# Kernel tuning notes

Hardware: AMD Instinct MI355X
Metric: run time of the kernel (lower is better)

Reference implementation:

```python
import jax, jax.numpy as jnp
import numpy as np

B, T, N, H = 512, 128, 256, 256  # batch, time_step, input_size, hidden_size


def setup_inputs() -> dict:
    key = jax.random.key(0)
    ks = jax.random.split(key, 8)
    s_lin = 1.0 / np.sqrt(T)
    s_ih = 1.0 / np.sqrt(H)
    return {
        "X": jax.random.normal(ks[0], (B, T, N), dtype=jnp.float32),
        "Wq": jax.random.uniform(ks[1], (T, T), jnp.float32, -s_lin, s_lin),
        "Wk": jax.random.uniform(ks[2], (T, T), jnp.float32, -s_lin, s_lin),
        "Wv": jax.random.uniform(ks[3], (T, T), jnp.float32, -s_lin, s_lin),
        "W_ih": jax.random.uniform(ks[4], (4 * H, N), jnp.float32, -s_ih, s_ih),
        "W_hh": jax.random.uniform(ks[5], (4 * H, H), jnp.float32, -s_ih, s_ih),
        "b_ih": jax.random.uniform(ks[6], (4 * H,), jnp.float32, -s_ih, s_ih),
        "b_hh": jax.random.uniform(ks[7], (4 * H,), jnp.float32, -s_ih, s_ih),
    }


def _forward(X, Wq, Wk, Wv, W_ih, W_hh, b_ih, b_hh):
    b, t, n = X.shape
    Xp = jnp.swapaxes(X, 1, 2)  # (B, N, T)
    Q = Xp @ Wq.T               # (B, N, T)
    K = Xp @ Wk.T               # (B, N, T)
    V = Xp @ Wv.T               # (B, N, T)
    # QK[b,i,j] = sum_t Q[b,i,t] * K[b,j,t]; scale by sqrt(N)
    scores = jnp.einsum('bit,bjt->bij', Q, K) / jnp.sqrt(jnp.float32(n))
    A = jax.nn.softmax(scores, axis=-1)          # (B, N, N)
    Xa = jnp.einsum('bij,bjt->bit', A, V)        # (B, N, T)
    Xa = jnp.swapaxes(Xa, 1, 2)                  # (B, T, N)

    h0 = jnp.zeros((b, W_hh.shape[1]), X.dtype)
    c0 = h0

    def step(carry, x_t):
        h, c = carry
        gates = x_t @ W_ih.T + b_ih + h @ W_hh.T + b_hh  # (B, 4H)
        i, f, g, o = jnp.split(gates, 4, axis=-1)         # PyTorch gate order
        i = jax.nn.sigmoid(i)
        f = jax.nn.sigmoid(f)
        g = jnp.tanh(g)
        o = jax.nn.sigmoid(o)
        c = f * c + i * g
        h = o * jnp.tanh(c)
        return (h, c), h

    _, hs = jax.lax.scan(step, (h0, c0), jnp.swapaxes(Xa, 0, 1))  # (T, B, H)
    return jnp.swapaxes(hs, 0, 1)  # (B, T, H)


def reference(X, Wq, Wk, Wv, W_ih, W_hh, b_ih, b_hh):
    return _forward(X, Wq, Wk, Wv, W_ih, W_hh, b_ih, b_hh)
```

## Files before the change

kernel.cpp:

```cpp
#include <hip/hip_runtime.h>
#include <hip/hip_bf16.h>
#include <stdint.h>


#define DI __device__ __forceinline__

typedef __attribute__((ext_vector_type(8))) short bf16x8;
typedef __attribute__((ext_vector_type(4))) short short4v;
typedef __attribute__((ext_vector_type(4))) float f32x4;
typedef __attribute__((ext_vector_type(4))) int int4v;

union U8 { bf16x8 v; short4v h[2]; int4v i; };

DI unsigned short f2bf(float x){
  union { float f; unsigned u; } v; v.f = x;
  unsigned r = v.u + 0x7fffu + ((v.u >> 16) & 1u);
  return (unsigned short)(r >> 16);
}
DI float bf2f(unsigned short x){
  union { unsigned u; float f; } v; v.u = ((unsigned)x) << 16; return v.f;
}
DI float rcp_(float x){ return __builtin_amdgcn_rcpf(x); }
DI float sigm(float x){ return rcp_(1.0f + __expf(-x)); }
DI float tanhf_(float x){ return 1.0f - 2.0f * rcp_(1.0f + __expf(2.0f * x)); }

#define BB 512
#define TT 128
#define NN 256
#define HH 256

__global__ void k_prep3(const float* __restrict__ Wq, const float* __restrict__ Wk,
                        const float* __restrict__ Wv, const float* __restrict__ Wih,
                        const float* __restrict__ Whh,
                        const float* __restrict__ bih, const float* __restrict__ bhh,
                        unsigned short* __restrict__ wqb, unsigned short* __restrict__ wkb,
                        unsigned short* __restrict__ wvb,
                        unsigned short* __restrict__ wihf, unsigned short* __restrict__ whhf,
                        float* __restrict__ bias, int* __restrict__ flags){
  int bx = blockIdx.x;
  if (bx < 64){
    int i = bx * 256 + threadIdx.x;
    wqb[i] = f2bf(Wq[i]); wkb[i] = f2bf(Wk[i]); wvb[i] = f2bf(Wv[i]);
    if (i < 1024) bias[i] = bih[i] + bhh[i];
    if (i < 256) flags[i] = 0;
    return;
  }
  const float* W = (bx < 96) ? Whh : Wih;
  unsigned short* w_f = (bx < 96) ? whhf : wihf;
  int idx = ((bx < 96) ? (bx - 64) : (bx - 96)) * 256 + threadIdx.x;
  int j = idx >> 3, kk = idx & 7;
  const float* src = W + j * 256 + kk * 32;
  unsigned short o[32];
  #pragma unroll
  for (int g = 0; g < 4; ++g)
    #pragma unroll
    for (int e = 0; e < 4; ++e){
      o[g * 8 + e]     = f2bf(src[4 * g + e]);
      o[g * 8 + 4 + e] = f2bf(src[16 + 4 * g + e]);
    }
  int4v* dst = (int4v*)((char*)w_f + j * 512 + kk * 64);
  #pragma unroll
  for (int q = 0; q < 4; ++q) dst[q] = *(int4v*)(o + q * 8);
}

__global__ __launch_bounds__(256) void k_qkv2(const float* __restrict__ X,
      const unsigned short* __restrict__ Wqb, const unsigned short* __restrict__ Wkb,
      const unsigned short* __restrict__ Wvb,
      unsigned short* __restrict__ Qo, unsigned short* __restrict__ Ko,
      unsigned short* __restrict__ Vo){
  __shared__ __align__(16) char smem[98816];
  char* As2 = smem;
  float* tile = (float*)(smem + 32768);
  char* Bs = smem + 32768;
  char* Os = smem + 65536;
  int bid = blockIdx.x;
  int b = bid >> 1, nh = bid & 1;
  int n0 = nh * 128;
  int m0 = b * 256 + n0;
  int tid = threadIdx.x;

  {
    int nl = tid & 127, tg = tid >> 7;
    const float* src = X + (size_t)b * TT * NN + n0 + nl;
    #pragma unroll
    for (int r = 0; r < 64; ++r){
      int t = r * 2 + tg;
      tile[t * 129 + nl] = src[(size_t)t * NN];
    }
  }
  __syncthreads();
  {
    int tpos = tid & 31, nrow = tid >> 5;
    #pragma unroll
    for (int rr = 0; rr < 16; ++rr){
      int n = rr * 8 + nrow;
      int t0 = tpos * 4;
      short4v v = { (short)f2bf(tile[(t0    ) * 129 + n]),
                    (short)f2bf(tile[(t0 + 1) * 129 + n]),
                    (short)f2bf(tile[(t0 + 2) * 129 + n]),
                    (short)f2bf(tile[(t0 + 3) * 129 + n]) };
      *(short4v*)(As2 + n * 256 + ((t0 * 2) ^ ((n & 7) << 4))) = v;
    }
  }

  int lane = tid & 63, wv = tid >> 6;
  int wr = wv >> 1, wc = wv & 1;
  int l15 = lane & 15, g = lane >> 4;
  f32x4 zro = {0.f, 0.f, 0.f, 0.f};

  #pragma unroll 1
  for (int mode = 0; mode < 3; ++mode){
    const unsigned short* W = (mode == 0) ? Wqb : ((mode == 1) ? Wkb : Wvb);
    __syncthreads();
    #pragma unroll
    for (int it = 0; it < 16; ++it){
      int c = it * 256 + tid;
      int j = c >> 5;
      int kc = (c & 31) << 2;
      short4v v = *(const short4v*)(W + j * 128 + kc);
      *(short4v*)(Bs + j * 256 + ((kc * 2) ^ ((j & 7) << 4))) = v;
    }
    __syncthreads();
    f32x4 acc[4][4];
    #pragma unroll
    for (int a = 0; a < 4; ++a)
      #pragma unroll
      for (int bq = 0; bq < 4; ++bq) acc[a][bq] = zro;
    #pragma unroll
    for (int ks = 0; ks < 4; ++ks){
      U8 af[4];
      #pragma unroll
      for (int mt = 0; mt < 4; ++mt){
        int ar = wr * 64 + mt * 16 + l15;
        const char* ab = As2 + ar * 256;
        int sw = (ar & 7) << 4;
        af[mt].h[0] = *(const short4v*)(ab + ((ks * 64 + 8 * g) ^ sw));
        af[mt].h[1] = *(const short4v*)(ab + ((ks * 64 + 8 * g + 32) ^ sw));
      }
      #pragma unroll
      for (int nt = 0; nt < 4; ++nt){
        int jr = wc * 64 + nt * 16 + l15;
        const char* bb = Bs + jr * 256;
        int kb = ks * 64 + 8 * g, sw = (jr & 7) << 4;
        U8 bf;
        bf.h[0] = *(const short4v*)(bb + (kb ^ sw));
        bf.h[1] = *(const short4v*)(bb + ((kb + 32) ^ sw));
        #pragma unroll
        for (int mt = 0; mt < 4; ++mt)
          acc[mt][nt] = __builtin_amdgcn_mfma_f32_16x16x32_bf16(af[mt].v, bf.v, acc[mt][nt], 0, 0, 0);
      }
    }
    float scale = (mode == 0) ? 0.0625f : 1.0f;
    #pragma unroll
    for (int mt = 0; mt < 4; ++mt)
      #pragma unroll
      for (int nt = 0; nt < 4; ++nt)
        #pragma unroll
        for (int r = 0; r < 4; ++r){
          int row = wr * 64 + mt * 16 + g * 4 + r;
          int col = wc * 64 + nt * 16 + l15;
          unsigned short hv = f2bf(acc[mt][nt][r] * scale);
          int addr = (mode == 2) ? (col * 256 + ((row * 2) ^ ((col & 7) << 4)))
                                 : (row * 256 + ((col * 2) ^ ((row & 7) << 4)));
          *(unsigned short*)(Os + addr) = hv;
        }
    __syncthreads();
    int orow = tid >> 1, oseg = tid & 1;
    const char* srcrow = Os + orow * 256;
    unsigned short* dst;
    if (mode == 2){
      dst = Vo + ((size_t)b * 128 + orow) * 256 + n0 + oseg * 64;
    } else {
      dst = ((mode == 0) ? Qo : Ko) + (size_t)(m0 + orow) * 128 + oseg * 64;
    }
    #pragma unroll
    for (int c = 0; c < 8; ++c){
      int kb = oseg * 128 + c * 16;
      *(int4v*)((char*)dst + c * 16) = *(const int4v*)(srcrow + (kb ^ ((orow & 7) << 4)));
    }
  }
}

__global__ __launch_bounds__(512) void k_attn2(const unsigned short* __restrict__ Q,
        const unsigned short* __restrict__ K, const unsigned short* __restrict__ Vt,
        unsigned short* __restrict__ Xa){
  __shared__ __align__(16) char smem[131072 + 512];
  char* Qs = smem;
  char* Ks = smem + 32768;
  char* Ps = smem;
  char* Vs = smem + 65536;
  float* rden = (float*)(smem + 131072);
  int b = blockIdx.y, i0 = blockIdx.x * 128;
  int tid = threadIdx.x, lane = tid & 63, wv = tid >> 6;
  int l15 = lane & 15, g = lane >> 4;

  {
    int row = tid >> 2, q = tid & 3;
    const char* src = (const char*)(Q + ((size_t)b * 256 + i0 + row) * 128) + q * 64;
    char* dstr = Qs + row * 256;
    int sw = (row & 7) << 4;
    #pragma unroll
    for (int c = 0; c < 4; ++c){
      int kb = q * 64 + c * 16;
      *(int4v*)(dstr + (kb ^ sw)) = *(const int4v*)(src + c * 16);
    }
  }
  {
    int row = tid >> 1, half = tid & 1;
    const char* src = (const char*)(K + ((size_t)b * 256 + row) * 128) + half * 128;
    char* dstr = Ks + row * 256;
    int sw = (row & 7) << 4;
    #pragma unroll
    for (int c = 0; c < 8; ++c){
      int kb = half * 128 + c * 16;
      *(int4v*)(dstr + (kb ^ sw)) = *(const int4v*)(src + c * 16);
    }
  }
  __syncthreads();

  f32x4 zro = {0.f, 0.f, 0.f, 0.f};
  f32x4 acc[16];
  #pragma unroll
  for (int nt = 0; nt < 16; ++nt) acc[nt] = zro;
  #pragma unroll
  for (int kk = 0; kk < 4; ++kk){
    int ar = wv * 16 + l15;
    const char* ab = Qs + ar * 256;
    int kb = kk * 64 + 8 * g, swa = (ar & 7) << 4;
    U8 a;
    a.h[0] = *(const short4v*)(ab + (kb ^ swa));
    a.h[1] = *(const short4v*)(ab + ((kb + 32) ^ swa));
    #pragma unroll
    for (int nt = 0; nt < 16; ++nt){
      int jr = nt * 16 + l15;
      const char* bb = Ks + jr * 256;
      int swb = (jr & 7) << 4;
      U8 bf;
      bf.h[0] = *(const short4v*)(bb + (kb ^ swb));
      bf.h[1] = *(const short4v*)(bb + ((kb + 32) ^ swb));
      acc[nt] = __builtin_amdgcn_mfma_f32_16x16x32_bf16(a.v, bf.v, acc[nt], 0, 0, 0);
    }
  }
  float mx[4], sm[4];
  #pragma unroll
  for (int r = 0; r < 4; ++r){
    float m = acc[0][r];
    #pragma unroll
    for (int nt = 1; nt < 16; ++nt) m = fmaxf(m, acc[nt][r]);
    #pragma unroll
    for (int s = 1; s < 16; s <<= 1) m = fmaxf(m, __shfl_xor(m, s));
    mx[r] = m;
  }
  #pragma unroll
  for (int r = 0; r < 4; ++r){
    float s = 0.f;
    #pragma unroll
    for (int nt = 0; nt < 16; ++nt){
      float p = __expf(acc[nt][r] - mx[r]);
      acc[nt][r] = p; s += p;
    }
    #pragma unroll
    for (int sd = 1; sd < 16; sd <<= 1) s += __shfl_xor(s, sd);
    sm[r] = s;
  }
  __syncthreads();
  #pragma unroll
  for (int nt = 0; nt < 16; ++nt)
    #pragma unroll
    for (int r = 0; r < 4; ++r){
      int ir = wv * 16 + g * 4 + r;
      *(unsigned short*)(Ps + ir * 512 + ((nt * 16 + l15) * 2 ^ ((ir & 7) << 4))) = f2bf(acc[nt][r]);
    }
  #pragma unroll
  for (int r = 0; r < 4; ++r)
    if (l15 == r) rden[wv * 16 + g * 4 + r] = rcp_(sm[r]);
  {
    int row = tid >> 2, q = tid & 3;
    const char* src = (const char*)(Vt + ((size_t)b * 128 + row) * 256) + q * 128;
    char* dstr = Vs + row * 512;
    int sw = (row & 7) << 4;
    #pragma unroll
    for (int c = 0; c < 8; ++c){
      int jb = q * 128 + c * 16;
      *(int4v*)(dstr + (jb ^ sw)) = *(const int4v*)(src + c * 16);
    }
  }
  __syncthreads();

  f32x4 acc2[8];
  #pragma unroll
  for (int nt = 0; nt < 8; ++nt) acc2[nt] = zro;
  #pragma unroll
  for (int kk = 0; kk < 8; ++kk){
    int kb = kk * 64 + 8 * g;
    U8 bfr[8];
    #pragma unroll
    for (int nt = 0; nt < 8; ++nt){
      int ir = nt * 16 + l15;
      const char* pb = Ps + ir * 512;
      int sw = (ir & 7) << 4;
      bfr[nt].h[0] = *(const short4v*)(pb + (kb ^ sw));
      bfr[nt].h[1] = *(const short4v*)(pb + ((kb + 32) ^ sw));
    }
    int tr = wv * 16 + l15;
    const char* ab = Vs + tr * 512;
    int sw = (tr & 7) << 4;
    U8 a;
    a.h[0] = *(const short4v*)(ab + (kb ^ sw));
    a.h[1] = *(const short4v*)(ab + ((kb + 32) ^ sw));
    #pragma unroll
    for (int nt = 0; nt < 8; ++nt)
      acc2[nt] = __builtin_amdgcn_mfma_f32_16x16x32_bf16(a.v, bfr[nt].v, acc2[nt], 0, 0, 0);
  }
  #pragma unroll
  for (int nt = 0; nt < 8; ++nt){
    float rd = rden[nt * 16 + l15];
    #pragma unroll
    for (int r = 0; r < 4; ++r){
      int t = wv * 16 + g * 4 + r;
      int i = i0 + nt * 16 + l15;
      Xa[((size_t)b * 128 + t) * 256 + i] = f2bf(acc2[nt][r] * rd);
    }
  }
}

__global__ __launch_bounds__(512, 2) void k_lstm9(const unsigned short* __restrict__ Xa,
        const unsigned short* __restrict__ whh_f, const unsigned short* __restrict__ wih_f,
        const float* __restrict__ bias, float* __restrict__ out,
        unsigned int* __restrict__ hbuf, int* __restrict__ flags){
  __shared__ __align__(16) char smem[131072 + 8192 + 8192 + 8448];
  char* WI = smem;
  char* HS = smem + 131072;
  char* XS = smem + 139264;
  float* GS = (float*)(smem + 147456);
  int tid = threadIdx.x, lane = tid & 63, wv = tid >> 6;
  int l15 = lane & 15, g = lane >> 4;
  int bid = blockIdx.x;
  int x = bid & 7, q = bid >> 3;
  int y = q >> 2, m = q & 3;
  int grp = y * 8 + x;
  int b0 = grp * 8;
  int c0 = m * 64;
  int tb = tid >> 6, tc = tid & 63;

  U8 breg[2][8];
  #pragma unroll
  for (int nt = 0; nt < 2; ++nt){
    int jl = wv * 32 + nt * 16 + l15;
    int jg = (jl >> 6) * 256 + c0 + (jl & 63);
    #pragma unroll
    for (int kk = 0; kk < 8; ++kk)
      breg[nt][kk].i = *(const int4v*)((const char*)whh_f + (size_t)jg * 512 + kk * 64 + g * 16);
  }
  {
    int jl = tid >> 1, hq = (tid & 1) * 16;
    int jg = (jl >> 6) * 256 + c0 + (jl & 63);
    const char* src = (const char*)wih_f + (size_t)jg * 512;
    char* dst = WI + jl * 512;
    int sx = jl & 7;
    #pragma unroll
    for (int c2 = 0; c2 < 16; ++c2){
      int c = hq + c2;
      *(int4v*)(dst + ((c ^ sx) << 4)) = *(const int4v*)(src + c * 16);
    }
  }
  { int4v z = {0,0,0,0}; *(int4v*)(HS + tid * 16) = z; }
  if (tid < 256){ int4v z = {0,0,0,0}; *(int4v*)(XS + 4096 + tid * 16) = z; }
  {
    short4v v = *(const short4v*)(Xa + ((size_t)(b0 + tb) * 128) * 256 + tc * 4);
    *(short4v*)(XS + tb * 512 + ((tc * 8) ^ ((tb & 7) << 3))) = v;
  }
  float bs0 = bias[      c0 + tc], bs1 = bias[256 + c0 + tc];
  float bs2 = bias[512 + c0 + tc], bs3 = bias[768 + c0 + tc];
  float cst = 0.f;
  __syncthreads();

  int swA = (l15 & 7) << 3;
  const char* hsrow = HS + l15 * 512;
  const char* xsrow = XS + l15 * 512;
  const char* wib0 = WI + (wv * 32 + l15) * 512;
  const char* wib1 = WI + (wv * 32 + 16 + l15) * 512;
  int keep = g >> 1;
  f32x4 zro = {0.f, 0.f, 0.f, 0.f};

  f32x4 accX[2] = {zro, zro};
  #pragma unroll
  for (int kk = 0; kk < 8; ++kk){
    U8 a2, w0, w1;
    a2.h[0] = *(const short4v*)(xsrow + ((kk * 64 + 8 * g) ^ swA));
    a2.h[1] = *(const short4v*)(xsrow + ((kk * 64 + 32 + 8 * g) ^ swA));
    int cx = ((kk * 4 + g) ^ (l15 & 7)) << 4;
    w0.i = *(const int4v*)(wib0 + cx);
    w1.i = *(const int4v*)(wib1 + cx);
    accX[0] = __builtin_amdgcn_mfma_f32_16x16x32_bf16(a2.v, w0.v, accX[0], 0, 0, 0);
    accX[1] = __builtin_amdgcn_mfma_f32_16x16x32_bf16(a2.v, w1.v, accX[1], 0, 0, 0);
  }

  #pragma unroll 1
  for (int t = 0; t < 128; ++t){
    short4v xan = {0, 0, 0, 0};
    if (t < 127)
      xan = *(const short4v*)(Xa + ((size_t)(b0 + tb) * 128 + (t + 1)) * 256 + tc * 4);
    f32x4 acc[2] = {accX[0], accX[1]};
    #pragma unroll
    for (int kk = 0; kk < 8; ++kk){
      U8 a;
      a.h[0] = *(const short4v*)(hsrow + ((kk * 64 + 8 * g) ^ swA));
      a.h[1] = *(const short4v*)(hsrow + ((kk * 64 + 32 + 8 * g) ^ swA));
      acc[0] = __builtin_amdgcn_mfma_f32_16x16x32_bf16(a.v, breg[0][kk].v, acc[0], 0, 0, 0);
      acc[1] = __builtin_amdgcn_mfma_f32_16x16x32_bf16(a.v, breg[1][kk].v, acc[1], 0, 0, 0);
    }
    #pragma unroll
    for (int r = 0; r < 4; ++r){
      float v0 = acc[0][r], v1 = acc[1][r];
      float kv = keep ? v1 : v0;
      float sv = keep ? v0 : v1;
      float val = kv + __shfl_xor(sv, 32);
      int jl = wv * 32 + keep * 16 + l15;
      int batch = (g & 1) * 4 + r;
      GS[batch * 264 + (jl >> 6) * 66 + (jl & 63)] = val;
    }
    __syncthreads();
    float gv0 = GS[tb * 264 +   0 + tc];
    float gv1 = GS[tb * 264 +  66 + tc];
    float gv2 = GS[tb * 264 + 132 + tc];
    float gv3 = GS[tb * 264 + 198 + tc];
    float gi = sigm(gv0 + bs0);
    float gf = sigm(gv1 + bs1);
    float gg = tanhf_(gv2 + bs2);
    float go = sigm(gv3 + bs3);
    float c = gf * cst + gi * gg;
    cst = c;
    float h = go * tanhf_(c);
    out[((size_t)(b0 + tb) * 128 + t) * 256 + c0 + tc] = h;
    if (t < 127){
      unsigned short hhi = f2bf(h);
      unsigned short hlo = f2bf(h - bf2f(hhi));
      unsigned int pk = (unsigned int)hhi | ((unsigned int)hlo << 16);
      unsigned int* hb = hbuf + ((size_t)grp * 2 + (t & 1)) * 2048;
      __hip_atomic_store(hb + tb * 256 + c0 + tc, pk, __ATOMIC_RELAXED, __HIP_MEMORY_SCOPE_AGENT);
      *(short4v*)(XS + tb * 512 + ((tc * 8) ^ ((tb & 7) << 3))) = xan;
      __syncthreads();
      if (tid == 0)
        __hip_atomic_store(&flags[grp * 4 + m], t + 1, __ATOMIC_RELAXED, __HIP_MEMORY_SCOPE_AGENT);
      accX[0] = zro; accX[1] = zro;
      #pragma unroll
      for (int kk = 0; kk < 8; ++kk){
        U8 a2, w0, w1;
        a2.h[0] = *(const short4v*)(xsrow + ((kk * 64 + 8 * g) ^ swA));
        a2.h[1] = *(const short4v*)(xsrow + ((kk * 64 + 32 + 8 * g) ^ swA));
        int cx = ((kk * 4 + g) ^ (l15 & 7)) << 4;
        w0.i = *(const int4v*)(wib0 + cx);
        w1.i = *(const int4v*)(wib1 + cx);
        accX[0] = __builtin_amdgcn_mfma_f32_16x16x32_bf16(a2.v, w0.v, accX[0], 0, 0, 0);
        accX[1] = __builtin_amdgcn_mfma_f32_16x16x32_bf16(a2.v, w1.v, accX[1], 0, 0, 0);
      }
      if (lane >= 1 && lane <= 3){
        int pl = lane - 1;
        int pslot = pl + (pl >= m ? 1 : 0);
        while (__hip_atomic_load(&flags[grp * 4 + pslot], __ATOMIC_RELAXED,
                                 __HIP_MEMORY_SCOPE_AGENT) <= t){}
      }
      {
        int bb = tid >> 6, cg = tid & 63;
        const unsigned long long* sp =
            (const unsigned long long*)(hb + bb * 256 + cg * 4);
        unsigned long long w0 = __hip_atomic_load(sp,     __ATOMIC_RELAXED, __HIP_MEMORY_SCOPE_AGENT);
        unsigned long long w1 = __hip_atomic_load(sp + 1, __ATOMIC_RELAXED, __HIP_MEMORY_SCOPE_AGENT);
        unsigned int u0 = (unsigned int)w0, u1 = (unsigned int)(w0 >> 32);
        unsigned int u2 = (unsigned int)w1, u3 = (unsigned int)(w1 >> 32);
        short4v hiv = { (short)(u0 & 0xffff), (short)(u1 & 0xffff),
                        (short)(u2 & 0xffff), (short)(u3 & 0xffff) };
        short4v lov = { (short)(u0 >> 16), (short)(u1 >> 16),
                        (short)(u2 >> 16), (short)(u3 >> 16) };
        int sw = (bb & 7) << 3;
        int cb = (cg * 8) ^ sw;
        *(short4v*)(HS + bb * 512 + cb) = hiv;
        *(short4v*)(HS + (bb + 8) * 512 + cb) = lov;
      }
      __syncthreads();
    }
  }
}

extern "C" void kernel_launch(void* const* d_in, const int* in_sizes, int n_in,
                              void* d_out, int out_size, void* d_ws, size_t ws_size,
                              hipStream_t stream){
  (void)in_sizes; (void)n_in; (void)out_size; (void)ws_size;
  const float* X   = (const float*)d_in[0];
  const float* Wq  = (const float*)d_in[1];
  const float* Wk  = (const float*)d_in[2];
  const float* Wv  = (const float*)d_in[3];
  const float* Wih = (const float*)d_in[4];
  const float* Whh = (const float*)d_in[5];
  const float* bih = (const float*)d_in[6];
  const float* bhh = (const float*)d_in[7];
  float* out = (float*)d_out;
  char* ws = (char*)d_ws;

  const size_t SZ = 33554432ULL;
  unsigned short* p_q  = (unsigned short*)ws;
  unsigned short* p_k  = (unsigned short*)(ws + SZ);
  unsigned short* p_vt = (unsigned short*)(ws + 2 * SZ);
  unsigned short* p_xa = (unsigned short*)(ws + 3 * SZ);
  char* p = ws + 4 * SZ;
  unsigned short* p_wqb = (unsigned short*)p; p += 32768;
  unsigned short* p_wkb = (unsigned short*)p; p += 32768;
  unsigned short* p_wvb = (unsigned short*)p; p += 32768;
  unsigned short* p_whhf= (unsigned short*)p; p += 524288;
  unsigned short* p_wihf= (unsigned short*)p; p += 524288;
  float* p_bias = (float*)p; p += 4096;
  unsigned int* p_hbuf = (unsigned int*)p; p += 1048576;
  int* p_flags = (int*)p;

  k_prep3<<<128, 256, 0, stream>>>(Wq, Wk, Wv, Wih, Whh, bih, bhh,
                                   p_wqb, p_wkb, p_wvb, p_wihf, p_whhf,
                                   p_bias, p_flags);
  k_qkv2<<<1024, 256, 0, stream>>>(X, p_wqb, p_wkb, p_wvb, p_q, p_k, p_vt);
  k_attn2<<<dim3(2, 512), 512, 0, stream>>>(p_q, p_k, p_vt, p_xa);
  k_lstm9<<<256, 512, 0, stream>>>(p_xa, p_whhf, p_wihf, p_bias, out, p_hbuf, p_flags);
}
```

Baseline: 514.4 us.

## Use per-wave inter-block flags and 16-byte LDS fragment layout in LSTM

Replaces the single per-block completion flag with one flag per wavefront. Each wave publishes its h slice right after its own stores drain, and consumers wait only on the matching wave's flags in peer blocks, so signaling no longer sits behind a block barrier. The H and X staging buffers in LDS are also relaid so each MFMA A-fragment is one 16-byte read instead of two 8-byte reads. This costs eight times more flags and more polling traffic, and adds an explicit vmcnt wait before each flag store.

```diff
diff --git a/kernel.cpp b/kernel.cpp
--- a/kernel.cpp
+++ b/kernel.cpp
@@ -42,7 +42,7 @@
     int i = bx * 256 + threadIdx.x;
     wqb[i] = f2bf(Wq[i]); wkb[i] = f2bf(Wk[i]); wvb[i] = f2bf(Wv[i]);
     if (i < 1024) bias[i] = bih[i] + bhh[i];
-    if (i < 256) flags[i] = 0;
+    if (i < 2048) flags[i] = 0;
     return;
   }
   const float* W = (bx < 96) ? Whh : Wih;
@@ -324,7 +324,7 @@
   }
 }
 
-__global__ __launch_bounds__(512, 2) void k_lstm9(const unsigned short* __restrict__ Xa,
+__global__ __launch_bounds__(512, 2) void k_lstm10(const unsigned short* __restrict__ Xa,
         const unsigned short* __restrict__ whh_f, const unsigned short* __restrict__ wih_f,
         const float* __restrict__ bias, float* __restrict__ out,
         unsigned int* __restrict__ hbuf, int* __restrict__ flags){
@@ -342,6 +342,8 @@
   int b0 = grp * 8;
   int c0 = m * 64;
   int tb = tid >> 6, tc = tid & 63;
+  int f_kk = tc >> 3, f_g = tc & 3, f_hf = (tc >> 2) & 1;
+  int f_off = f_hf * 8;
 
   U8 breg[2][8];
   #pragma unroll
@@ -368,18 +370,18 @@
   if (tid < 256){ int4v z = {0,0,0,0}; *(int4v*)(XS + 4096 + tid * 16) = z; }
   {
     short4v v = *(const short4v*)(Xa + ((size_t)(b0 + tb) * 128) * 256 + tc * 4);
-    *(short4v*)(XS + tb * 512 + ((tc * 8) ^ ((tb & 7) << 3))) = v;
+    *(short4v*)(XS + tb * 512 + (((f_kk * 4 + f_g) ^ (tb & 7)) << 4) + f_off) = v;
   }
   float bs0 = bias[      c0 + tc], bs1 = bias[256 + c0 + tc];
   float bs2 = bias[512 + c0 + tc], bs3 = bias[768 + c0 + tc];
   float cst = 0.f;
   __syncthreads();
 
-  int swA = (l15 & 7) << 3;
   const char* hsrow = HS + l15 * 512;
   const char* xsrow = XS + l15 * 512;
   const char* wib0 = WI + (wv * 32 + l15) * 512;
   const char* wib1 = WI + (wv * 32 + 16 + l15) * 512;
+  int sxa = l15 & 7;
   int keep = g >> 1;
   f32x4 zro = {0.f, 0.f, 0.f, 0.f};
 
@@ -387,9 +389,8 @@
   #pragma unroll
   for (int kk = 0; kk < 8; ++kk){
     U8 a2, w0, w1;
-    a2.h[0] = *(const short4v*)(xsrow + ((kk * 64 + 8 * g) ^ swA));
-    a2.h[1] = *(const short4v*)(xsrow + ((kk * 64 + 32 + 8 * g) ^ swA));
-    int cx = ((kk * 4 + g) ^ (l15 & 7)) << 4;
+    int cx = ((kk * 4 + g) ^ sxa) << 4;
+    a2.i = *(const int4v*)(xsrow + cx);
     w0.i = *(const int4v*)(wib0 + cx);
     w1.i = *(const int4v*)(wib1 + cx);
     accX[0] = __builtin_amdgcn_mfma_f32_16x16x32_bf16(a2.v, w0.v, accX[0], 0, 0, 0);
@@ -405,8 +406,7 @@
     #pragma unroll
     for (int kk = 0; kk < 8; ++kk){
       U8 a;
-      a.h[0] = *(const short4v*)(hsrow + ((kk * 64 + 8 * g) ^ swA));
-      a.h[1] = *(const short4v*)(hsrow + ((kk * 64 + 32 + 8 * g) ^ swA));
+      a.i = *(const int4v*)(hsrow + (((kk * 4 + g) ^ sxa) << 4));
       acc[0] = __builtin_amdgcn_mfma_f32_16x16x32_bf16(a.v, breg[0][kk].v, acc[0], 0, 0, 0);
       acc[1] = __builtin_amdgcn_mfma_f32_16x16x32_bf16(a.v, breg[1][kk].v, acc[1], 0, 0, 0);
     }
@@ -439,17 +439,18 @@
       unsigned int pk = (unsigned int)hhi | ((unsigned int)hlo << 16);
       unsigned int* hb = hbuf + ((size_t)grp * 2 + (t & 1)) * 2048;
       __hip_atomic_store(hb + tb * 256 + c0 + tc, pk, __ATOMIC_RELAXED, __HIP_MEMORY_SCOPE_AGENT);
-      *(short4v*)(XS + tb * 512 + ((tc * 8) ^ ((tb & 7) << 3))) = xan;
+      *(short4v*)(XS + tb * 512 + (((f_kk * 4 + f_g) ^ (tb & 7)) << 4) + f_off) = xan;
+      asm volatile("s_waitcnt vmcnt(0)" ::: "memory");
+      if (lane == 0)
+        __hip_atomic_store(&flags[grp * 32 + m * 8 + wv], t + 1,
+                           __ATOMIC_RELAXED, __HIP_MEMORY_SCOPE_AGENT);
       __syncthreads();
-      if (tid == 0)
-        __hip_atomic_store(&flags[grp * 4 + m], t + 1, __ATOMIC_RELAXED, __HIP_MEMORY_SCOPE_AGENT);
       accX[0] = zro; accX[1] = zro;
       #pragma unroll
       for (int kk = 0; kk < 8; ++kk){
         U8 a2, w0, w1;
-        a2.h[0] = *(const short4v*)(xsrow + ((kk * 64 + 8 * g) ^ swA));
-        a2.h[1] = *(const short4v*)(xsrow + ((kk * 64 + 32 + 8 * g) ^ swA));
-        int cx = ((kk * 4 + g) ^ (l15 & 7)) << 4;
+        int cx = ((kk * 4 + g) ^ sxa) << 4;
+        a2.i = *(const int4v*)(xsrow + cx);
         w0.i = *(const int4v*)(wib0 + cx);
         w1.i = *(const int4v*)(wib1 + cx);
         accX[0] = __builtin_amdgcn_mfma_f32_16x16x32_bf16(a2.v, w0.v, accX[0], 0, 0, 0);
@@ -458,11 +459,11 @@
       if (lane >= 1 && lane <= 3){
         int pl = lane - 1;
         int pslot = pl + (pl >= m ? 1 : 0);
-        while (__hip_atomic_load(&flags[grp * 4 + pslot], __ATOMIC_RELAXED,
+        while (__hip_atomic_load(&flags[grp * 32 + pslot * 8 + wv], __ATOMIC_RELAXED,
                                  __HIP_MEMORY_SCOPE_AGENT) <= t){}
       }
       {
-        int bb = tid >> 6, cg = tid & 63;
+        int bb = wv, cg = tc;
         const unsigned long long* sp =
             (const unsigned long long*)(hb + bb * 256 + cg * 4);
         unsigned long long w0 = __hip_atomic_load(sp,     __ATOMIC_RELAXED, __HIP_MEMORY_SCOPE_AGENT);
@@ -473,10 +474,9 @@
                         (short)(u2 & 0xffff), (short)(u3 & 0xffff) };
         short4v lov = { (short)(u0 >> 16), (short)(u1 >> 16),
                         (short)(u2 >> 16), (short)(u3 >> 16) };
-        int sw = (bb & 7) << 3;
-        int cb = (cg * 8) ^ sw;
-        *(short4v*)(HS + bb * 512 + cb) = hiv;
-        *(short4v*)(HS + (bb + 8) * 512 + cb) = lov;
+        int coff = (((f_kk * 4 + f_g) ^ (bb & 7)) << 4) + f_off;
+        *(short4v*)(HS + bb * 512 + coff) = hiv;
+        *(short4v*)(HS + (bb + 8) * 512 + coff) = lov;
       }
       __syncthreads();
     }
@@ -518,5 +518,5 @@
                                    p_bias, p_flags);
   k_qkv2<<<1024, 256, 0, stream>>>(X, p_wqb, p_wkb, p_wvb, p_q, p_k, p_vt);
   k_attn2<<<dim3(2, 512), 512, 0, stream>>>(p_q, p_k, p_vt, p_xa);
-  k_lstm9<<<256, 512, 0, stream>>>(p_xa, p_whhf, p_wihf, p_bias, out, p_hbuf, p_flags);
-}
+  k_lstm10<<<256, 512, 0, stream>>>(p_xa, p_whhf, p_wihf, p_bias, out, p_hbuf, p_flags);
+}
```

Result: no change. 515.8 us (+0.3%).
